# Kernel tuning notes

Hardware: AMD Instinct MI355X
Metric: run time of the kernel (lower is better)

Reference implementation:

```python
import jax, jax.numpy as jnp
import numpy as np

N_HEAD, D_K, D_V = 8, 32, 32
ATTN_MAX_DIST = 3
LN_EPS = 1e-6


def _layernorm(x, w, b):
    mu = jnp.mean(x, axis=-1, keepdims=True)
    var = jnp.mean(jnp.square(x - mu), axis=-1, keepdims=True)
    return (x - mu) * jax.lax.rsqrt(var + LN_EPS) * w + b


def setup_inputs() -> dict:
    key = jax.random.key(0)
    ks = jax.random.split(key, 8)
    B, E, D, PMAX = 4, 1500, 256, 5
    x = jax.random.normal(ks[0], (B, D, E), dtype=jnp.float32)
    dist_matrices = jax.random.randint(ks[1], (B, E, E), 0, 11, dtype=jnp.int32)
    s = 0.02
    Wq = jax.random.normal(ks[2], (D, N_HEAD * D_K), dtype=jnp.float32) * s
    Wk = jax.random.normal(ks[3], (D, N_HEAD * D_K), dtype=jnp.float32) * s
    Wv = jax.random.normal(ks[4], (D, N_HEAD * D_V), dtype=jnp.float32) * s
    Wfc = jax.random.normal(ks[5], (N_HEAD * D_V, D), dtype=jnp.float32) * s
    ln_w = jnp.ones((D,), dtype=jnp.float32)
    ln_b = jnp.zeros((D,), dtype=jnp.float32)
    base_rpr = jax.random.normal(ks[6], (PMAX + 1, D_K), dtype=jnp.float32) * s
    return {"x": x, "dist_matrices": dist_matrices, "Wq": Wq, "Wk": Wk,
            "Wv": Wv, "Wfc": Wfc, "ln_w": ln_w, "ln_b": ln_b, "base_rpr": base_rpr}


def reference(x, dist_matrices, Wq, Wk, Wv, Wfc, ln_w, ln_b, base_rpr):
    B, D, E = x.shape
    H, DK, DV = N_HEAD, D_K, D_V
    s = jnp.transpose(x, (0, 2, 1))          # [B, E, D]
    residual = s
    # NOTE: in the original, only q is layer-normed; k and v use raw input.
    qn = _layernorm(s, ln_w, ln_b)
    q = (qn @ Wq).reshape(B, E, H, DK).transpose(0, 2, 1, 3)   # [B,H,E,DK]
    k = (s @ Wk).reshape(B, E, H, DK).transpose(0, 2, 1, 3)
    v = (s @ Wv).reshape(B, E, H, DV).transpose(0, 2, 1, 3)
    qs = q / jnp.sqrt(jnp.asarray(DK, q.dtype))
    attn1 = jnp.einsum('bhqd,bhkd->bhqk', qs, k)               # [B,H,E,E]
    q_dot_rpr = jnp.einsum('bhqd,pd->bhqp', qs, base_rpr)      # [B,H,E,P+1]
    max_neighbor = base_rpr.shape[0] - 1
    idx = jnp.minimum(dist_matrices, max_neighbor)             # [B,E,E]
    idx4 = jnp.broadcast_to(idx[:, None], (B, H, E, E))
    attn2 = jnp.take_along_axis(q_dot_rpr, idx4, axis=-1)      # gather bias per edge pair
    attn = attn1 + attn2
    mask = dist_matrices <= ATTN_MAX_DIST                      # [B,E,E] local attention mask
    attn = jnp.where(mask[:, None], attn, jnp.asarray(-1e9, attn.dtype))
    attn = jax.nn.softmax(attn, axis=-1)                       # dropout=eval -> identity
    out = jnp.einsum('bhqk,bhkd->bhqd', attn, v)               # [B,H,E,DV]
    out = out.transpose(0, 2, 1, 3).reshape(B, E, H * DV)
    out = out @ Wfc + residual                                 # [B,E,D]
    x_out = jnp.transpose(out, (0, 2, 1))                      # [B,D,E]
    # attention-per-edge statistic (no grads in original: detached)
    m = mask[:, None].astype(attn.dtype)                       # [B,1,E,E]
    attn_sum = jnp.sum(jax.lax.stop_gradient(attn) * m, axis=(1, 2))  # [B,E]
    valid = jnp.sum(m, axis=(1, 2))                            # [B,E] (broadcasted over heads)
    attn_per_edge = attn_sum / valid
    return (x_out, attn, attn_per_edge)
```

## Files before the change

### kernel.cpp

```cpp
#include <hip/hip_runtime.h>


#define E_ 1500
#define D_ 256
#define HH 8
#define BB 4
#define MM (BB * E_)
#define KT_ 64
#define NKT_ 24

typedef float f32x4 __attribute__((ext_vector_type(4)));
typedef short short8 __attribute__((ext_vector_type(8)));

static __device__ inline unsigned short f2bf(float f) {
  unsigned u = __float_as_uint(f);
  unsigned r = (u + 0x7fff + ((u >> 16) & 1)) >> 16;
  return (unsigned short)r;
}
static __device__ inline float bf2f(unsigned short u) {
  return __uint_as_float(((unsigned)u) << 16);
}

__global__ __launch_bounds__(256) void t0_transpose(const float* __restrict__ x,
                                                    float* __restrict__ xt,
                                                    unsigned short* __restrict__ xtb) {
  __shared__ float tl[32][33];
  const int b = blockIdx.z;
  const int dt = blockIdx.x * 32;
  const int et = blockIdx.y * 32;
  const int tx = threadIdx.x, ty = threadIdx.y;
#pragma unroll
  for (int j = 0; j < 4; j++) {
    int d = dt + ty + j * 8;
    int e = et + tx;
    float v = 0.f;
    if (e < E_) v = x[(size_t)b * D_ * E_ + (size_t)d * E_ + e];
    tl[ty + j * 8][tx] = v;
  }
  __syncthreads();
#pragma unroll
  for (int j = 0; j < 4; j++) {
    int e = et + ty + j * 8;
    int d = dt + tx;
    if (e < E_) {
      float v = tl[tx][ty + j * 8];
      size_t idx = ((size_t)b * E_ + e) * D_ + d;
      xt[idx] = v;
      xtb[idx] = f2bf(v);
    }
  }
}

__global__ __launch_bounds__(256) void t1_wt(const float* __restrict__ Wq,
                                             const float* __restrict__ Wk,
                                             const float* __restrict__ Wv,
                                             const float* __restrict__ Wfc,
                                             unsigned short* __restrict__ WT) {
  __shared__ float tl[32][33];
  const int mat = blockIdx.z;
  const float* W = (mat == 0) ? Wq : (mat == 1) ? Wk : (mat == 2) ? Wv : Wfc;
  const int kt = blockIdx.x * 32, nt = blockIdx.y * 32;
  const int tx = threadIdx.x, ty = threadIdx.y;
#pragma unroll
  for (int j = 0; j < 4; j++)
    tl[ty + j * 8][tx] = W[(size_t)(kt + ty + j * 8) * 256 + nt + tx];
  __syncthreads();
#pragma unroll
  for (int j = 0; j < 4; j++)
    WT[(size_t)mat * 65536 + (size_t)(nt + ty + j * 8) * 256 + kt + tx] =
        f2bf(tl[tx][ty + j * 8]);
}

__global__ __launch_bounds__(256) void k1_ln(const float* __restrict__ xt,
                                             const float* __restrict__ lnw,
                                             const float* __restrict__ lnb,
                                             unsigned short* __restrict__ qnb) {
  const int m = blockIdx.x;
  const int t = threadIdx.x;
  float v = xt[(size_t)m * D_ + t];
  float s = v, s2 = v * v;
#pragma unroll
  for (int o = 1; o < 64; o <<= 1) {
    s += __shfl_xor(s, o);
    s2 += __shfl_xor(s2, o);
  }
  __shared__ float ps[4], ps2[4], mv[2];
  const int w = t >> 6;
  if ((t & 63) == 0) { ps[w] = s; ps2[w] = s2; }
  __syncthreads();
  if (t == 0) {
    float ts = ps[0] + ps[1] + ps[2] + ps[3];
    float ts2 = ps2[0] + ps2[1] + ps2[2] + ps2[3];
    float mu = ts * (1.f / 256.f);
    float var = ts2 * (1.f / 256.f) - mu * mu;
    mv[0] = mu;
    mv[1] = rsqrtf(var + 1e-6f);
  }
  __syncthreads();
  qnb[(size_t)m * D_ + t] = f2bf((v - mv[0]) * mv[1] * lnw[t] + lnb[t]);
}

__global__ __launch_bounds__(256) void kproj(
    const unsigned short* __restrict__ xtb, const unsigned short* __restrict__ qnb,
    const unsigned short* __restrict__ WT, unsigned short* __restrict__ qb,
    unsigned short* __restrict__ kb, unsigned short* __restrict__ vb) {
  const int mat = blockIdx.y >> 2;
  const int n0 = (blockIdx.y & 3) * 64;
  const int m0 = blockIdx.x * 64;
  const int t = threadIdx.x;
  const int w = t >> 6, l = t & 63, quad = l >> 4, l15 = l & 15;
  const unsigned short* A = (mat == 0) ? qnb : xtb;
  const unsigned short* B = WT + (size_t)mat * 65536;
  unsigned short* dst = (mat == 0) ? qb : ((mat == 1) ? kb : vb);
  const float scale = (mat == 0) ? 0.17677669529663687f : 1.0f;

  int mrow = m0 + w * 16 + l15;
  if (mrow > MM - 1) mrow = MM - 1;
  short8 af[8];
#pragma unroll
  for (int kc = 0; kc < 8; kc++)
    af[kc] = *(const short8*)(A + (size_t)mrow * 256 + kc * 32 + quad * 8);

#pragma unroll
  for (int ntile = 0; ntile < 4; ntile++) {
    const int n = n0 + ntile * 16 + l15;
    f32x4 acc = {0.f, 0.f, 0.f, 0.f};
#pragma unroll
    for (int kc = 0; kc < 8; kc++) {
      short8 bf = *(const short8*)(B + (size_t)n * 256 + kc * 32 + quad * 8);
      acc = __builtin_amdgcn_mfma_f32_16x16x32_bf16(af[kc], bf, acc, 0, 0, 0);
    }
#pragma unroll
    for (int r = 0; r < 4; r++) {
      int m = m0 + w * 16 + quad * 4 + r;
      if (m < MM) dst[(size_t)m * 256 + n] = f2bf(acc[r] * scale);
    }
  }
}

__global__ __launch_bounds__(512, 2) void k2_attn(
    const unsigned short* __restrict__ qb, const unsigned short* __restrict__ kb,
    const unsigned short* __restrict__ vb, const int* __restrict__ dist,
    const float* __restrict__ rpr, float* __restrict__ attn,
    unsigned short* __restrict__ aob, float* __restrict__ asum,
    float* __restrict__ validf) {
  __shared__ unsigned short vT[2][8][2312];
  __shared__ unsigned short pS[8][2312];
  __shared__ int distT[2][2816];
  __shared__ float qdrS[8][32][4];
  __shared__ float rinvS[8][32];

  const int blk = blockIdx.x;
  const int b = blk / 47;
  const int qt = blk % 47;
  const int q0 = qt * 32;
  const int t = threadIdx.x;
  const int w = t >> 6, l = t & 63, quad = l >> 4, l15 = l & 15;

#pragma unroll
  for (int ii = 0; ii < 2; ii++) {
    int id = t + ii * 512;
    int h = id >> 7, rem = id & 127, q = rem >> 2, p = rem & 3;
    int qg = q0 + q;
    float s = 0.f;
    if (qg < E_) {
      const unsigned short* qp = qb + ((size_t)(b * E_ + qg)) * 256 + h * 32;
      for (int d = 0; d < 32; d++) s += bf2f(qp[d]) * rpr[p * 32 + d];
    }
    qdrS[h][q][p] = s;
  }

  short8 aq[2];
#pragma unroll
  for (int qs = 0; qs < 2; qs++) {
    int qg = q0 + qs * 16 + l15;
    if (qg > E_ - 1) qg = E_ - 1;
    aq[qs] = *(const short8*)(qb + ((size_t)(b * E_ + qg)) * 256 + w * 32 + quad * 8);
  }

  float rs[2][4] = {{0.f, 0.f, 0.f, 0.f}, {0.f, 0.f, 0.f, 0.f}};
  f32x4 accPV[2][2];
#pragma unroll
  for (int qs = 0; qs < 2; qs++)
#pragma unroll
    for (int dv = 0; dv < 2; dv++) {
      f32x4 z = {0.f, 0.f, 0.f, 0.f};
      accPV[qs][dv] = z;
    }

  short8 kregA[4], kregB[4];

  auto loadD = [&](int kt) -> int4 {
    int qrow = t >> 4, c0 = (t & 15) * 4;
    int qg = q0 + qrow;
    int rq = qg < E_ ? qg : E_ - 1;
    int cb = kt * KT_ + c0;
    int cc2 = cb <= E_ - 4 ? cb : E_ - 4;
    return *(const int4*)(dist + ((size_t)b * E_ + rq) * (size_t)E_ + cc2);
  };
  auto writeD = [&](int kt, int buf, int4 d4) {
    int qrow = t >> 4, c0 = (t & 15) * 4;
    int qg = q0 + qrow;
    int cb = kt * KT_ + c0;
    int da[4] = {d4.x, d4.y, d4.z, d4.w};
#pragma unroll
    for (int j = 0; j < 4; j++) {
      int ok = (qg < E_) & ((cb + j) < E_);
      distT[buf][(c0 + j) * 44 + qrow] = ok ? da[j] : 8;
    }
  };
  auto loadV = [&](int kt, uint4 (&vr)[4]) {
    const int r = t >> 3, hh = t & 7;
    const int kg = kt * KT_ + r;
    const uint4 z = {0u, 0u, 0u, 0u};
    if (kg < E_) {
      const unsigned short* vp = vb + ((size_t)(b * E_ + kg)) * 256 + hh * 32;
      vr[0] = *(const uint4*)(vp);
      vr[1] = *(const uint4*)(vp + 8);
      vr[2] = *(const uint4*)(vp + 16);
      vr[3] = *(const uint4*)(vp + 24);
    } else {
      vr[0] = z; vr[1] = z; vr[2] = z; vr[3] = z;
    }
  };
  auto writeV = [&](int buf, const uint4 (&vr)[4]) {
    const int r = t >> 3, hh = t & 7;
    union { uint4 u[4]; unsigned short s[32]; } vv;
    vv.u[0] = vr[0]; vv.u[1] = vr[1]; vv.u[2] = vr[2]; vv.u[3] = vr[3];
#pragma unroll
    for (int j = 0; j < 32; j++) vT[buf][hh][j * 72 + r] = vv.s[j];
  };
  auto loadK = [&](int kt, short8 (&kr)[4]) {
#pragma unroll
    for (int ks = 0; ks < 4; ks++) {
      int kg = kt * KT_ + ks * 16 + l15;
      if (kg > E_ - 1) kg = E_ - 1;
      kr[ks] = *(const short8*)(kb + ((size_t)(b * E_ + kg)) * 256 + w * 32 + quad * 8);
    }
  };

  auto body1 = [&](int kt, short8 (&kcur)[4], short8 (&knxt)[4], int cur) {
    const int k0 = kt * KT_;
    const int nxt = cur ^ 1;
    const bool pf = (kt + 1) < NKT_;
    int4 d4;
    uint4 vr[4];
    if (pf) {
      d4 = loadD(kt + 1);
      loadV(kt + 1, vr);
      loadK(kt + 1, knxt);
    }
    int cc[4] = {0, 0, 0, 0};
#pragma unroll
    for (int qs = 0; qs < 2; qs++) {
#pragma unroll
      for (int ks = 0; ks < 4; ks++) {
        f32x4 z = {0.f, 0.f, 0.f, 0.f};
        f32x4 c = __builtin_amdgcn_mfma_f32_16x16x32_bf16(aq[qs], kcur[ks], z, 0, 0, 0);
        int4 dd4 = *(const int4*)&distT[cur][(ks * 16 + l15) * 44 + qs * 16 + quad * 4];
        int da[4] = {dd4.x, dd4.y, dd4.z, dd4.w};
#pragma unroll
        for (int r = 0; r < 4; r++) {
          int ql = qs * 16 + quad * 4 + r;
          float e = 0.f;
          if (da[r] <= 3) e = __expf(c[r] + qdrS[w][ql][da[r] & 3]);
          rs[qs][r] += e;
          pS[w][ql * 72 + ks * 16 + l15] = f2bf(e);
        }
        if (w == 0)
          cc[ks] += (da[0] <= 3) + (da[1] <= 3) + (da[2] <= 3) + (da[3] <= 3);
      }
    }
    if (w == 0) {
#pragma unroll
      for (int ks = 0; ks < 4; ks++) {
        int v = cc[ks];
        v += __shfl_xor(v, 16);
        v += __shfl_xor(v, 32);
        int kcol = k0 + ks * 16 + l15;
        if (quad == 0 && kcol < E_) atomicAdd(validf + b * E_ + kcol, (float)v);
      }
    }
#pragma unroll
    for (int kc = 0; kc < 2; kc++) {
      short8 bv0 = *(const short8*)&vT[cur][w][(l15) * 72 + kc * 32 + quad * 8];
      short8 bv1 = *(const short8*)&vT[cur][w][(16 + l15) * 72 + kc * 32 + quad * 8];
#pragma unroll
      for (int qs = 0; qs < 2; qs++) {
        short8 ap = *(const short8*)&pS[w][(qs * 16 + l15) * 72 + kc * 32 + quad * 8];
        accPV[qs][0] = __builtin_amdgcn_mfma_f32_16x16x32_bf16(ap, bv0, accPV[qs][0], 0, 0, 0);
        accPV[qs][1] = __builtin_amdgcn_mfma_f32_16x16x32_bf16(ap, bv1, accPV[qs][1], 0, 0, 0);
      }
    }
    if (pf) {
      writeD(kt + 1, nxt, d4);
      writeV(nxt, vr);
    }
    __syncthreads();
  };

  auto body2 = [&](int kt, short8 (&kcur)[4], short8 (&knxt)[4], int cur) {
    const int k0 = kt * KT_;
    const int nxt = cur ^ 1;
    const bool pf = (kt + 1) < NKT_;
    int4 d4;
    if (pf) {
      d4 = loadD(kt + 1);
      loadK(kt + 1, knxt);
    }
    float ca[4] = {0.f, 0.f, 0.f, 0.f};
    const size_t abase = ((size_t)(b * HH + w)) * E_;
#pragma unroll
    for (int qs = 0; qs < 2; qs++) {
#pragma unroll
      for (int ks = 0; ks < 4; ks++) {
        f32x4 z = {0.f, 0.f, 0.f, 0.f};
        f32x4 c = __builtin_amdgcn_mfma_f32_16x16x32_bf16(aq[qs], kcur[ks], z, 0, 0, 0);
        int4 dd4 = *(const int4*)&distT[cur][(ks * 16 + l15) * 44 + qs * 16 + quad * 4];
        int da[4] = {dd4.x, dd4.y, dd4.z, dd4.w};
        int kcol = k0 + ks * 16 + l15;
#pragma unroll
        for (int r = 0; r < 4; r++) {
          int ql = qs * 16 + quad * 4 + r;
          float p = 0.f;
          if (da[r] <= 3)
            p = __expf(c[r] + qdrS[w][ql][da[r] & 3]) * rinvS[w][ql];
          ca[ks] += p;
          int qg = q0 + ql;
          if (qg < E_ && kcol < E_) attn[(abase + qg) * E_ + kcol] = p;
        }
      }
    }
#pragma unroll
    for (int ks = 0; ks < 4; ks++) {
      float v = ca[ks];
      v += __shfl_xor(v, 16);
      v += __shfl_xor(v, 32);
      int kcol = k0 + ks * 16 + l15;
      if (quad == 0 && kcol < E_) atomicAdd(asum + b * E_ + kcol, v);
    }
    if (pf) writeD(kt + 1, nxt, d4);
    __syncthreads();
  };

  {
    int4 d4 = loadD(0);
    uint4 vr[4];
    loadV(0, vr);
    loadK(0, kregA);
    writeD(0, 0, d4);
    writeV(0, vr);
  }
  __syncthreads();
  for (int kt = 0; kt < NKT_; kt += 2) {
    body1(kt, kregA, kregB, 0);
    body1(kt + 1, kregB, kregA, 1);
  }

#pragma unroll
  for (int qs = 0; qs < 2; qs++)
#pragma unroll
    for (int r = 0; r < 4; r++) {
      float v = rs[qs][r];
      v += __shfl_xor(v, 1);
      v += __shfl_xor(v, 2);
      v += __shfl_xor(v, 4);
      v += __shfl_xor(v, 8);
      if (l15 == 0) rinvS[w][qs * 16 + quad * 4 + r] = v;
    }
  __syncthreads();
  if (t < 256) {
    int h = t >> 5, q = t & 31;
    float s = rinvS[h][q];
    rinvS[h][q] = (s > 0.f) ? 1.f / s : 0.f;
  }
  __syncthreads();

#pragma unroll
  for (int qs = 0; qs < 2; qs++)
#pragma unroll
    for (int dv = 0; dv < 2; dv++) {
      f32x4 a = accPV[qs][dv];
#pragma unroll
      for (int r = 0; r < 4; r++) {
        int ql = qs * 16 + quad * 4 + r;
        int qg = q0 + ql;
        if (qg < E_)
          aob[((size_t)(b * E_ + qg)) * 256 + w * 32 + dv * 16 + l15] =
              f2bf(a[r] * rinvS[w][ql]);
      }
    }

  {
    int4 d4 = loadD(0);
    loadK(0, kregA);
    writeD(0, 0, d4);
  }
  __syncthreads();
  for (int kt = 0; kt < NKT_; kt += 2) {
    body2(kt, kregA, kregB, 0);
    body2(kt + 1, kregB, kregA, 1);
  }
}

__global__ __launch_bounds__(256) void k_fc(const unsigned short* __restrict__ aob,
                                            const unsigned short* __restrict__ WT,
                                            const float* __restrict__ x,
                                            float* __restrict__ xout) {
  const int n0 = blockIdx.y * 64;
  const int m0 = blockIdx.x * 64;
  const int t = threadIdx.x;
  const int w = t >> 6, l = t & 63, quad = l >> 4, l15 = l & 15;
  const unsigned short* B = WT + (size_t)3 * 65536;

  int mrow = m0 + w * 16 + l15;
  if (mrow > MM - 1) mrow = MM - 1;
  short8 af[8];
#pragma unroll
  for (int kc = 0; kc < 8; kc++)
    af[kc] = *(const short8*)(aob + (size_t)mrow * 256 + kc * 32 + quad * 8);

#pragma unroll
  for (int ntile = 0; ntile < 4; ntile++) {
    const int nc = n0 + ntile * 16 + l15;
    f32x4 acc = {0.f, 0.f, 0.f, 0.f};
#pragma unroll
    for (int kc = 0; kc < 8; kc++) {
      short8 bf = *(const short8*)(B + (size_t)nc * 256 + kc * 32 + quad * 8);
      acc = __builtin_amdgcn_mfma_f32_16x16x32_bf16(af[kc], bf, acc, 0, 0, 0);
    }
    int m = m0 + w * 16 + quad * 4;
    if (m < MM) {
      int bb = m / E_, e = m - bb * E_;
      size_t idx = ((size_t)bb * 256 + nc) * E_ + e;
      float4 rx = *(const float4*)(x + idx);
      *(float4*)(xout + idx) = make_float4(acc[0] + rx.x, acc[1] + rx.y,
                                           acc[2] + rx.z, acc[3] + rx.w);
    }
  }
}

__global__ __launch_bounds__(256) void k5_div(const float* __restrict__ asum,
                                              const float* __restrict__ validf,
                                              float* __restrict__ ape) {
  int i = blockIdx.x * 256 + threadIdx.x;
  if (i < BB * E_) ape[i] = asum[i] / validf[i];
}

extern "C" void kernel_launch(void* const* d_in, const int* in_sizes, int n_in,
                              void* d_out, int out_size, void* d_ws,
                              size_t ws_size, hipStream_t stream) {
  const float* x = (const float*)d_in[0];
  const int* dist = (const int*)d_in[1];
  const float* Wq = (const float*)d_in[2];
  const float* Wk = (const float*)d_in[3];
  const float* Wv = (const float*)d_in[4];
  const float* Wfc = (const float*)d_in[5];
  const float* lnw = (const float*)d_in[6];
  const float* lnb = (const float*)d_in[7];
  const float* rpr = (const float*)d_in[8];

  float* out0 = (float*)d_out;
  float* attn = out0 + 1536000;
  float* ape = out0 + 73536000;

  float* ws = (float*)d_ws;
  float* xt = ws;
  unsigned short* xtb = (unsigned short*)(ws + 1536000);
  unsigned short* qnb = (unsigned short*)(ws + 2304000);
  unsigned short* qb = (unsigned short*)(ws + 3072000);
  unsigned short* kb = (unsigned short*)(ws + 3840000);
  unsigned short* vb = (unsigned short*)(ws + 4608000);
  unsigned short* aob = (unsigned short*)(ws + 5376000);
  unsigned short* WT = (unsigned short*)(ws + 6144000);
  float* asum = ws + 6275072;
  float* validf = ws + 6281072;

  hipMemsetAsync(asum, 0, 12000 * sizeof(float), stream);

  t0_transpose<<<dim3(8, 47, 4), dim3(32, 8), 0, stream>>>(x, xt, xtb);
  t1_wt<<<dim3(8, 8, 4), dim3(32, 8), 0, stream>>>(Wq, Wk, Wv, Wfc, WT);
  k1_ln<<<MM, 256, 0, stream>>>(xt, lnw, lnb, qnb);
  kproj<<<dim3(94, 12), 256, 0, stream>>>(xtb, qnb, WT, qb, kb, vb);
  k2_attn<<<188, 512, 0, stream>>>(qb, kb, vb, dist, rpr, attn, aob, asum,
                                   validf);
  k_fc<<<dim3(94, 4), 256, 0, stream>>>(aob, WT, x, out0);
  k5_div<<<24, 256, 0, stream>>>(asum, validf, ape);
}
```

Baseline: 629.0 us.

## Pack distance matrix into LDS nibbles, pre-transpose V, fuse transpose with layernorm

```diff
diff --git a/kernel.cpp b/kernel.cpp
--- a/kernel.cpp
+++ b/kernel.cpp
@@ -6,11 +6,12 @@
 #define HH 8
 #define BB 4
 #define MM (BB * E_)
-#define KT_ 64
 #define NKT_ 24
+#define VROW 1536
 
 typedef float f32x4 __attribute__((ext_vector_type(4)));
 typedef short short8 __attribute__((ext_vector_type(8)));
+typedef unsigned uint2v __attribute__((ext_vector_type(2)));
 
 static __device__ inline unsigned short f2bf(float f) {
   unsigned u = __float_as_uint(f);
@@ -21,32 +22,56 @@
   return __uint_as_float(((unsigned)u) << 16);
 }
 
-__global__ __launch_bounds__(256) void t0_transpose(const float* __restrict__ x,
-                                                    float* __restrict__ xt,
-                                                    unsigned short* __restrict__ xtb) {
-  __shared__ float tl[32][33];
-  const int b = blockIdx.z;
-  const int dt = blockIdx.x * 32;
-  const int et = blockIdx.y * 32;
-  const int tx = threadIdx.x, ty = threadIdx.y;
-#pragma unroll
-  for (int j = 0; j < 4; j++) {
-    int d = dt + ty + j * 8;
-    int e = et + tx;
-    float v = 0.f;
-    if (e < E_) v = x[(size_t)b * D_ * E_ + (size_t)d * E_ + e];
-    tl[ty + j * 8][tx] = v;
+__global__ __launch_bounds__(256) void t0ln(const float* __restrict__ x,
+                                            const float* __restrict__ lnw,
+                                            const float* __restrict__ lnb,
+                                            unsigned short* __restrict__ xtb,
+                                            unsigned short* __restrict__ qnb) {
+  __shared__ float tl[32][257];
+  const int b = blockIdx.y;
+  const int e0 = blockIdx.x * 32;
+  const int t = threadIdx.x;
+  const int tx = t & 31, ty8 = t >> 5;
+#pragma unroll
+  for (int dt = 0; dt < 8; dt++) {
+#pragma unroll
+    for (int j = 0; j < 4; j++) {
+      int d = dt * 32 + ty8 * 4 + j;
+      int e = e0 + tx;
+      float v = (e < E_) ? x[((size_t)b * D_ + d) * E_ + e] : 0.f;
+      tl[tx][d] = v;
+    }
   }
   __syncthreads();
-#pragma unroll
-  for (int j = 0; j < 4; j++) {
-    int e = et + ty + j * 8;
-    int d = dt + tx;
-    if (e < E_) {
-      float v = tl[tx][ty + j * 8];
-      size_t idx = ((size_t)b * E_ + e) * D_ + d;
-      xt[idx] = v;
-      xtb[idx] = f2bf(v);
+  const int er = t >> 3, seg = t & 7;
+  float s = 0.f, s2 = 0.f;
+#pragma unroll
+  for (int j = 0; j < 32; j++) {
+    float v = tl[er][seg + j * 8];
+    s += v;
+    s2 += v * v;
+  }
+  s += __shfl_xor(s, 1); s2 += __shfl_xor(s2, 1);
+  s += __shfl_xor(s, 2); s2 += __shfl_xor(s2, 2);
+  s += __shfl_xor(s, 4); s2 += __shfl_xor(s2, 4);
+  float mu = s * (1.f / 256.f);
+  float var = s2 * (1.f / 256.f) - mu * mu;
+  float rsig = rsqrtf(var + 1e-6f);
+  int eg = e0 + er;
+  if (eg < E_) {
+    size_t ro = ((size_t)b * E_ + eg) * 256;
+#pragma unroll
+    for (int g = 0; g < 4; g++) {
+      int d0 = seg * 32 + g * 8;
+      union { unsigned short u[8]; short8 v; } xs, qs8;
+#pragma unroll
+      for (int j = 0; j < 8; j++) {
+        float v = tl[er][d0 + j];
+        xs.u[j] = f2bf(v);
+        qs8.u[j] = f2bf((v - mu) * rsig * lnw[d0 + j] + lnb[d0 + j]);
+      }
+      *(short8*)(xtb + ro + d0) = xs.v;
+      *(short8*)(qnb + ro + d0) = qs8.v;
     }
   }
 }
@@ -71,39 +96,10 @@
         f2bf(tl[tx][ty + j * 8]);
 }
 
-__global__ __launch_bounds__(256) void k1_ln(const float* __restrict__ xt,
-                                             const float* __restrict__ lnw,
-                                             const float* __restrict__ lnb,
-                                             unsigned short* __restrict__ qnb) {
-  const int m = blockIdx.x;
-  const int t = threadIdx.x;
-  float v = xt[(size_t)m * D_ + t];
-  float s = v, s2 = v * v;
-#pragma unroll
-  for (int o = 1; o < 64; o <<= 1) {
-    s += __shfl_xor(s, o);
-    s2 += __shfl_xor(s2, o);
-  }
-  __shared__ float ps[4], ps2[4], mv[2];
-  const int w = t >> 6;
-  if ((t & 63) == 0) { ps[w] = s; ps2[w] = s2; }
-  __syncthreads();
-  if (t == 0) {
-    float ts = ps[0] + ps[1] + ps[2] + ps[3];
-    float ts2 = ps2[0] + ps2[1] + ps2[2] + ps2[3];
-    float mu = ts * (1.f / 256.f);
-    float var = ts2 * (1.f / 256.f) - mu * mu;
-    mv[0] = mu;
-    mv[1] = rsqrtf(var + 1e-6f);
-  }
-  __syncthreads();
-  qnb[(size_t)m * D_ + t] = f2bf((v - mv[0]) * mv[1] * lnw[t] + lnb[t]);
-}
-
 __global__ __launch_bounds__(256) void kproj(
     const unsigned short* __restrict__ xtb, const unsigned short* __restrict__ qnb,
     const unsigned short* __restrict__ WT, unsigned short* __restrict__ qb,
-    unsigned short* __restrict__ kb, unsigned short* __restrict__ vb) {
+    unsigned short* __restrict__ kb, unsigned short* __restrict__ vbt) {
   const int mat = blockIdx.y >> 2;
   const int n0 = (blockIdx.y & 3) * 64;
   const int m0 = blockIdx.x * 64;
@@ -111,7 +107,6 @@
   const int w = t >> 6, l = t & 63, quad = l >> 4, l15 = l & 15;
   const unsigned short* A = (mat == 0) ? qnb : xtb;
   const unsigned short* B = WT + (size_t)mat * 65536;
-  unsigned short* dst = (mat == 0) ? qb : ((mat == 1) ? kb : vb);
   const float scale = (mat == 0) ? 0.17677669529663687f : 1.0f;
 
   int mrow = m0 + w * 16 + l15;
@@ -130,25 +125,38 @@
       short8 bf = *(const short8*)(B + (size_t)n * 256 + kc * 32 + quad * 8);
       acc = __builtin_amdgcn_mfma_f32_16x16x32_bf16(af[kc], bf, acc, 0, 0, 0);
     }
-#pragma unroll
-    for (int r = 0; r < 4; r++) {
-      int m = m0 + w * 16 + quad * 4 + r;
-      if (m < MM) dst[(size_t)m * 256 + n] = f2bf(acc[r] * scale);
+    if (mat == 2) {
+      int m = m0 + w * 16 + quad * 4;
+      if (m < MM) {
+        int bb = m / E_, e0 = m - bb * E_;
+        uint2v uv;
+        uv.x = (unsigned)f2bf(acc[0]) | ((unsigned)f2bf(acc[1]) << 16);
+        uv.y = (unsigned)f2bf(acc[2]) | ((unsigned)f2bf(acc[3]) << 16);
+        *(uint2v*)(vbt + (size_t)((bb * 8 + (n >> 5)) * 32 + (n & 31)) * VROW +
+                   e0) = uv;
+      }
+    } else {
+      unsigned short* dst = (mat == 0) ? qb : kb;
+#pragma unroll
+      for (int r = 0; r < 4; r++) {
+        int m = m0 + w * 16 + quad * 4 + r;
+        if (m < MM) dst[(size_t)m * 256 + n] = f2bf(acc[r] * scale);
+      }
     }
   }
 }
 
 __global__ __launch_bounds__(512, 2) void k2_attn(
     const unsigned short* __restrict__ qb, const unsigned short* __restrict__ kb,
-    const unsigned short* __restrict__ vb, const int* __restrict__ dist,
+    const unsigned short* __restrict__ vbt, const int* __restrict__ dist,
     const float* __restrict__ rpr, float* __restrict__ attn,
     unsigned short* __restrict__ aob, float* __restrict__ asum,
     float* __restrict__ validf) {
-  __shared__ unsigned short vT[2][8][2312];
-  __shared__ unsigned short pS[8][2312];
-  __shared__ int distT[2][2816];
+  __shared__ __align__(16) unsigned short vT[2][8][32][72];
+  __shared__ __align__(16) unsigned short pS[8][2320];
+  __shared__ __align__(16) unsigned char distN[32][776];
   __shared__ float qdrS[8][32][4];
-  __shared__ float rinvS[8][32];
+  __shared__ float colacc[1544];
 
   const int blk = blockIdx.x;
   const int b = blk / 47;
@@ -156,6 +164,32 @@
   const int q0 = qt * 32;
   const int t = threadIdx.x;
   const int w = t >> 6, l = t & 63, quad = l >> 4, l15 = l & 15;
+
+  for (int idx = t; idx < 32 * 188; idx += 512) {
+    int row = idx / 188, wd = idx - row * 188;
+    int qg = q0 + row;
+    int k0 = wd * 8;
+    unsigned word = 0x88888888u;
+    if (qg < E_) {
+      const int* dp = dist + ((size_t)b * E_ + qg) * E_ + k0;
+      int4 a = *(const int4*)dp;
+      word = (unsigned)(a.x & 15) | ((unsigned)(a.y & 15) << 4) |
+             ((unsigned)(a.z & 15) << 8) | ((unsigned)(a.w & 15) << 12);
+      if (k0 + 8 <= E_) {
+        int4 c = *(const int4*)(dp + 4);
+        word |= ((unsigned)(c.x & 15) << 16) | ((unsigned)(c.y & 15) << 20) |
+                ((unsigned)(c.z & 15) << 24) | ((unsigned)(c.w & 15) << 28);
+      } else {
+        word |= 0x88880000u;
+      }
+    }
+    *(unsigned*)&distN[row][wd * 4] = word;
+  }
+  for (int idx = t; idx < 32 * 6; idx += 512) {
+    int row = idx / 6, wd = 188 + idx - (idx / 6) * 6;
+    *(unsigned*)&distN[row][wd * 4] = 0x88888888u;
+  }
+  for (int idx = t; idx < 1544; idx += 512) colacc[idx] = 0.f;
 
 #pragma unroll
   for (int ii = 0; ii < 2; ii++) {
@@ -178,113 +212,75 @@
     aq[qs] = *(const short8*)(qb + ((size_t)(b * E_ + qg)) * 256 + w * 32 + quad * 8);
   }
 
-  float rs[2][4] = {{0.f, 0.f, 0.f, 0.f}, {0.f, 0.f, 0.f, 0.f}};
-  f32x4 accPV[2][2];
-#pragma unroll
-  for (int qs = 0; qs < 2; qs++)
-#pragma unroll
-    for (int dv = 0; dv < 2; dv++) {
-      f32x4 z = {0.f, 0.f, 0.f, 0.f};
-      accPV[qs][dv] = z;
-    }
-
-  short8 kregA[4], kregB[4];
-
-  auto loadD = [&](int kt) -> int4 {
-    int qrow = t >> 4, c0 = (t & 15) * 4;
-    int qg = q0 + qrow;
-    int rq = qg < E_ ? qg : E_ - 1;
-    int cb = kt * KT_ + c0;
-    int cc2 = cb <= E_ - 4 ? cb : E_ - 4;
-    return *(const int4*)(dist + ((size_t)b * E_ + rq) * (size_t)E_ + cc2);
-  };
-  auto writeD = [&](int kt, int buf, int4 d4) {
-    int qrow = t >> 4, c0 = (t & 15) * 4;
-    int qg = q0 + qrow;
-    int cb = kt * KT_ + c0;
-    int da[4] = {d4.x, d4.y, d4.z, d4.w};
-#pragma unroll
-    for (int j = 0; j < 4; j++) {
-      int ok = (qg < E_) & ((cb + j) < E_);
-      distT[buf][(c0 + j) * 44 + qrow] = ok ? da[j] : 8;
+  const unsigned short* kbase = kb + (size_t)b * E_ * 256 + w * 32 + quad * 8;
+  const int vrr = t >> 1, vh = vrr >> 5, vdv = vrr & 31, vc0 = (t & 1) * 32;
+  const unsigned short* vsrc = vbt + (size_t)((b * 8 + vh) * 32 + vdv) * VROW + vc0;
+
+  auto loadK = [&](int kt, short8 (&kf)[4]) {
+#pragma unroll
+    for (int ks = 0; ks < 4; ks++) {
+      int kg = kt * 64 + ks * 16 + l15;
+      if (kg > E_ - 1) kg = E_ - 1;
+      kf[ks] = *(const short8*)(kbase + (size_t)kg * 256);
     }
   };
   auto loadV = [&](int kt, uint4 (&vr)[4]) {
-    const int r = t >> 3, hh = t & 7;
-    const int kg = kt * KT_ + r;
-    const uint4 z = {0u, 0u, 0u, 0u};
-    if (kg < E_) {
-      const unsigned short* vp = vb + ((size_t)(b * E_ + kg)) * 256 + hh * 32;
-      vr[0] = *(const uint4*)(vp);
-      vr[1] = *(const uint4*)(vp + 8);
-      vr[2] = *(const uint4*)(vp + 16);
-      vr[3] = *(const uint4*)(vp + 24);
-    } else {
-      vr[0] = z; vr[1] = z; vr[2] = z; vr[3] = z;
-    }
+#pragma unroll
+    for (int j = 0; j < 4; j++) vr[j] = *(const uint4*)(vsrc + kt * 64 + j * 8);
   };
   auto writeV = [&](int buf, const uint4 (&vr)[4]) {
-    const int r = t >> 3, hh = t & 7;
-    union { uint4 u[4]; unsigned short s[32]; } vv;
-    vv.u[0] = vr[0]; vv.u[1] = vr[1]; vv.u[2] = vr[2]; vv.u[3] = vr[3];
-#pragma unroll
-    for (int j = 0; j < 32; j++) vT[buf][hh][j * 72 + r] = vv.s[j];
+    uint4* dst = (uint4*)&vT[buf][vh][vdv][vc0];
+#pragma unroll
+    for (int j = 0; j < 4; j++) dst[j] = vr[j];
   };
-  auto loadK = [&](int kt, short8 (&kr)[4]) {
-#pragma unroll
-    for (int ks = 0; ks < 4; ks++) {
-      int kg = kt * KT_ + ks * 16 + l15;
-      if (kg > E_ - 1) kg = E_ - 1;
-      kr[ks] = *(const short8*)(kb + ((size_t)(b * E_ + kg)) * 256 + w * 32 + quad * 8);
-    }
-  };
-
-  auto body1 = [&](int kt, short8 (&kcur)[4], short8 (&knxt)[4], int cur) {
-    const int k0 = kt * KT_;
-    const int nxt = cur ^ 1;
-    const bool pf = (kt + 1) < NKT_;
-    int4 d4;
+
+  short8 kA[4], kB[4];
+  f32x4 accPV[2][2];
+#pragma unroll
+  for (int qs = 0; qs < 2; qs++)
+#pragma unroll
+    for (int dvh = 0; dvh < 2; dvh++) {
+      f32x4 z = {0.f, 0.f, 0.f, 0.f};
+      accPV[qs][dvh] = z;
+    }
+  float rs[2][4] = {{0.f, 0.f, 0.f, 0.f}, {0.f, 0.f, 0.f, 0.f}};
+
+  {
     uint4 vr[4];
-    if (pf) {
-      d4 = loadD(kt + 1);
-      loadV(kt + 1, vr);
-      loadK(kt + 1, knxt);
-    }
-    int cc[4] = {0, 0, 0, 0};
+    loadV(0, vr);
+    loadK(0, kA);
+    writeV(0, vr);
+  }
+  __syncthreads();
+
+  auto body1 = [&](int kt, short8 (&kf)[4], short8 (&kn)[4], int cur) {
+    const int ktn = (kt + 1 < NKT_) ? kt + 1 : kt;
+    uint4 vr[4];
+    loadV(ktn, vr);
+    loadK(ktn, kn);
+    const int kl0 = kt * 64;
 #pragma unroll
     for (int qs = 0; qs < 2; qs++) {
 #pragma unroll
       for (int ks = 0; ks < 4; ks++) {
         f32x4 z = {0.f, 0.f, 0.f, 0.f};
-        f32x4 c = __builtin_amdgcn_mfma_f32_16x16x32_bf16(aq[qs], kcur[ks], z, 0, 0, 0);
-        int4 dd4 = *(const int4*)&distT[cur][(ks * 16 + l15) * 44 + qs * 16 + quad * 4];
-        int da[4] = {dd4.x, dd4.y, dd4.z, dd4.w};
+        f32x4 c = __builtin_amdgcn_mfma_f32_16x16x32_bf16(aq[qs], kf[ks], z, 0, 0, 0);
+        const int kcol = kl0 + ks * 16 + l15;
 #pragma unroll
         for (int r = 0; r < 4; r++) {
           int ql = qs * 16 + quad * 4 + r;
+          int dd = (distN[ql][kcol >> 1] >> ((kcol & 1) * 4)) & 15;
           float e = 0.f;
-          if (da[r] <= 3) e = __expf(c[r] + qdrS[w][ql][da[r] & 3]);
+          if (dd <= 3) e = __expf(c[r] + qdrS[w][ql][dd & 3]);
           rs[qs][r] += e;
           pS[w][ql * 72 + ks * 16 + l15] = f2bf(e);
         }
-        if (w == 0)
-          cc[ks] += (da[0] <= 3) + (da[1] <= 3) + (da[2] <= 3) + (da[3] <= 3);
-      }
-    }
-    if (w == 0) {
-#pragma unroll
-      for (int ks = 0; ks < 4; ks++) {
-        int v = cc[ks];
-        v += __shfl_xor(v, 16);
-        v += __shfl_xor(v, 32);
-        int kcol = k0 + ks * 16 + l15;
-        if (quad == 0 && kcol < E_) atomicAdd(validf + b * E_ + kcol, (float)v);
       }
     }
 #pragma unroll
     for (int kc = 0; kc < 2; kc++) {
-      short8 bv0 = *(const short8*)&vT[cur][w][(l15) * 72 + kc * 32 + quad * 8];
-      short8 bv1 = *(const short8*)&vT[cur][w][(16 + l15) * 72 + kc * 32 + quad * 8];
+      short8 bv0 = *(const short8*)&vT[cur][w][l15][kc * 32 + quad * 8];
+      short8 bv1 = *(const short8*)&vT[cur][w][16 + l15][kc * 32 + quad * 8];
 #pragma unroll
       for (int qs = 0; qs < 2; qs++) {
         short8 ap = *(const short8*)&pS[w][(qs * 16 + l15) * 72 + kc * 32 + quad * 8];
@@ -292,71 +288,16 @@
         accPV[qs][1] = __builtin_amdgcn_mfma_f32_16x16x32_bf16(ap, bv1, accPV[qs][1], 0, 0, 0);
       }
     }
-    if (pf) {
-      writeD(kt + 1, nxt, d4);
-      writeV(nxt, vr);
-    }
+    writeV(cur ^ 1, vr);
     __syncthreads();
   };
 
-  auto body2 = [&](int kt, short8 (&kcur)[4], short8 (&knxt)[4], int cur) {
-    const int k0 = kt * KT_;
-    const int nxt = cur ^ 1;
-    const bool pf = (kt + 1) < NKT_;
-    int4 d4;
-    if (pf) {
-      d4 = loadD(kt + 1);
-      loadK(kt + 1, knxt);
-    }
-    float ca[4] = {0.f, 0.f, 0.f, 0.f};
-    const size_t abase = ((size_t)(b * HH + w)) * E_;
-#pragma unroll
-    for (int qs = 0; qs < 2; qs++) {
-#pragma unroll
-      for (int ks = 0; ks < 4; ks++) {
-        f32x4 z = {0.f, 0.f, 0.f, 0.f};
-        f32x4 c = __builtin_amdgcn_mfma_f32_16x16x32_bf16(aq[qs], kcur[ks], z, 0, 0, 0);
-        int4 dd4 = *(const int4*)&distT[cur][(ks * 16 + l15) * 44 + qs * 16 + quad * 4];
-        int da[4] = {dd4.x, dd4.y, dd4.z, dd4.w};
-        int kcol = k0 + ks * 16 + l15;
-#pragma unroll
-        for (int r = 0; r < 4; r++) {
-          int ql = qs * 16 + quad * 4 + r;
-          float p = 0.f;
-          if (da[r] <= 3)
-            p = __expf(c[r] + qdrS[w][ql][da[r] & 3]) * rinvS[w][ql];
-          ca[ks] += p;
-          int qg = q0 + ql;
-          if (qg < E_ && kcol < E_) attn[(abase + qg) * E_ + kcol] = p;
-        }
-      }
-    }
-#pragma unroll
-    for (int ks = 0; ks < 4; ks++) {
-      float v = ca[ks];
-      v += __shfl_xor(v, 16);
-      v += __shfl_xor(v, 32);
-      int kcol = k0 + ks * 16 + l15;
-      if (quad == 0 && kcol < E_) atomicAdd(asum + b * E_ + kcol, v);
-    }
-    if (pf) writeD(kt + 1, nxt, d4);
-    __syncthreads();
-  };
-
-  {
-    int4 d4 = loadD(0);
-    uint4 vr[4];
-    loadV(0, vr);
-    loadK(0, kregA);
-    writeD(0, 0, d4);
-    writeV(0, vr);
-  }
-  __syncthreads();
   for (int kt = 0; kt < NKT_; kt += 2) {
-    body1(kt, kregA, kregB, 0);
-    body1(kt + 1, kregB, kregA, 1);
-  }
-
+    body1(kt, kA, kB, 0);
+    body1(kt + 1, kB, kA, 1);
+  }
+
+  float rinv[2][4];
 #pragma unroll
   for (int qs = 0; qs < 2; qs++)
 #pragma unroll
@@ -366,47 +307,81 @@
       v += __shfl_xor(v, 2);
       v += __shfl_xor(v, 4);
       v += __shfl_xor(v, 8);
-      if (l15 == 0) rinvS[w][qs * 16 + quad * 4 + r] = v;
-    }
-  __syncthreads();
-  if (t < 256) {
-    int h = t >> 5, q = t & 31;
-    float s = rinvS[h][q];
-    rinvS[h][q] = (s > 0.f) ? 1.f / s : 0.f;
-  }
-  __syncthreads();
+      rinv[qs][r] = (v > 0.f) ? 1.f / v : 0.f;
+    }
 
 #pragma unroll
   for (int qs = 0; qs < 2; qs++)
 #pragma unroll
-    for (int dv = 0; dv < 2; dv++) {
-      f32x4 a = accPV[qs][dv];
+    for (int dvh = 0; dvh < 2; dvh++) {
+      f32x4 a = accPV[qs][dvh];
 #pragma unroll
       for (int r = 0; r < 4; r++) {
         int ql = qs * 16 + quad * 4 + r;
         int qg = q0 + ql;
         if (qg < E_)
-          aob[((size_t)(b * E_ + qg)) * 256 + w * 32 + dv * 16 + l15] =
-              f2bf(a[r] * rinvS[w][ql]);
-      }
-    }
-
-  {
-    int4 d4 = loadD(0);
-    loadK(0, kregA);
-    writeD(0, 0, d4);
-  }
+          aob[((size_t)(b * E_ + qg)) * 256 + w * 32 + dvh * 16 + l15] =
+              f2bf(a[r] * rinv[qs][r]);
+      }
+    }
+
+  if (w == 0) {
+    for (int c = l; c < E_; c += 64) {
+      int cnt = 0;
+#pragma unroll
+      for (int r = 0; r < 32; r++)
+        cnt += (((distN[r][c >> 1] >> ((c & 1) * 4)) & 15) <= 3);
+      atomicAdd(validf + b * E_ + c, 8.f * (float)cnt);
+    }
+  }
+
+  loadK(0, kA);
+  auto body2 = [&](int kt, short8 (&kf)[4], short8 (&kn)[4]) {
+    const int ktn = (kt + 1 < NKT_) ? kt + 1 : kt;
+    loadK(ktn, kn);
+    const int kl0 = kt * 64;
+#pragma unroll
+    for (int ks = 0; ks < 4; ks++) {
+      const int kcol = kl0 + ks * 16 + l15;
+      const bool kok = kcol < E_;
+      float cs = 0.f;
+#pragma unroll
+      for (int qs = 0; qs < 2; qs++) {
+        f32x4 z = {0.f, 0.f, 0.f, 0.f};
+        f32x4 c = __builtin_amdgcn_mfma_f32_16x16x32_bf16(aq[qs], kf[ks], z, 0, 0, 0);
+#pragma unroll
+        for (int r = 0; r < 4; r++) {
+          int ql = qs * 16 + quad * 4 + r;
+          int dd = (distN[ql][kcol >> 1] >> ((kcol & 1) * 4)) & 15;
+          float p = 0.f;
+          if (dd <= 3) p = __expf(c[r] + qdrS[w][ql][dd & 3]) * rinv[qs][r];
+          cs += p;
+          int qg = q0 + ql;
+          if (qg < E_ && kok)
+            attn[((size_t)(b * 8 + w) * E_ + qg) * E_ + kcol] = p;
+        }
+      }
+      cs += __shfl_xor(cs, 16);
+      cs += __shfl_xor(cs, 32);
+      if (quad == 0 && kok) atomicAdd(&colacc[kl0 + ks * 16 + l15], cs);
+    }
+  };
+
+  for (int kt = 0; kt < NKT_; kt += 2) {
+    body2(kt, kA, kB);
+    body2(kt + 1, kB, kA);
+  }
+
   __syncthreads();
-  for (int kt = 0; kt < NKT_; kt += 2) {
-    body2(kt, kregA, kregB, 0);
-    body2(kt + 1, kregB, kregA, 1);
-  }
+  for (int idx = t; idx < E_; idx += 512)
+    atomicAdd(asum + b * E_ + idx, colacc[idx]);
 }
 
 __global__ __launch_bounds__(256) void k_fc(const unsigned short* __restrict__ aob,
                                             const unsigned short* __restrict__ WT,
                                             const float* __restrict__ x,
                                             float* __restrict__ xout) {
+  __shared__ float tl[64][65];
   const int n0 = blockIdx.y * 64;
   const int m0 = blockIdx.x * 64;
   const int t = threadIdx.x;
@@ -422,20 +397,34 @@
 
 #pragma unroll
   for (int ntile = 0; ntile < 4; ntile++) {
-    const int nc = n0 + ntile * 16 + l15;
+    const int nl = ntile * 16 + l15;
     f32x4 acc = {0.f, 0.f, 0.f, 0.f};
 #pragma unroll
     for (int kc = 0; kc < 8; kc++) {
-      short8 bf = *(const short8*)(B + (size_t)nc * 256 + kc * 32 + quad * 8);
+      short8 bf = *(const short8*)(B + (size_t)(n0 + nl) * 256 + kc * 32 + quad * 8);
       acc = __builtin_amdgcn_mfma_f32_16x16x32_bf16(af[kc], bf, acc, 0, 0, 0);
     }
-    int m = m0 + w * 16 + quad * 4;
+    const int ml = w * 16 + quad * 4;
+#pragma unroll
+    for (int r = 0; r < 4; r++) tl[ml + r][nl] = acc[r];
+  }
+  __syncthreads();
+  const int nl = t >> 2;
+  const int e0l = (t & 3) * 16;
+  const int nc = n0 + nl;
+#pragma unroll
+  for (int i = 0; i < 4; i++) {
+    int m = m0 + e0l + i * 4;
     if (m < MM) {
-      int bb = m / E_, e = m - bb * E_;
+      int bb = m / E_;
+      int e = m - bb * E_;
       size_t idx = ((size_t)bb * 256 + nc) * E_ + e;
       float4 rx = *(const float4*)(x + idx);
-      *(float4*)(xout + idx) = make_float4(acc[0] + rx.x, acc[1] + rx.y,
-                                           acc[2] + rx.z, acc[3] + rx.w);
+      float4 v = make_float4(tl[e0l + i * 4 + 0][nl] + rx.x,
+                             tl[e0l + i * 4 + 1][nl] + rx.y,
+                             tl[e0l + i * 4 + 2][nl] + rx.z,
+                             tl[e0l + i * 4 + 3][nl] + rx.w);
+      *(float4*)(xout + idx) = v;
     }
   }
 }
@@ -465,24 +454,23 @@
   float* ape = out0 + 73536000;
 
   float* ws = (float*)d_ws;
-  float* xt = ws;
-  unsigned short* xtb = (unsigned short*)(ws + 1536000);
-  unsigned short* qnb = (unsigned short*)(ws + 2304000);
-  unsigned short* qb = (unsigned short*)(ws + 3072000);
-  unsigned short* kb = (unsigned short*)(ws + 3840000);
-  unsigned short* vb = (unsigned short*)(ws + 4608000);
-  unsigned short* aob = (unsigned short*)(ws + 5376000);
-  unsigned short* WT = (unsigned short*)(ws + 6144000);
-  float* asum = ws + 6275072;
-  float* validf = ws + 6281072;
+  unsigned short* xtb = (unsigned short*)ws;
+  unsigned short* qnb = (unsigned short*)(ws + 768000);
+  unsigned short* qb = (unsigned short*)(ws + 1536000);
+  unsigned short* kb = (unsigned short*)(ws + 2304000);
+  unsigned short* vbt = (unsigned short*)(ws + 3072000);
+  unsigned short* aob = (unsigned short*)(ws + 3858432);
+  unsigned short* WT = (unsigned short*)(ws + 4626432);
+  float* asum = ws + 4757504;
+  float* validf = ws + 4763504;
 
   hipMemsetAsync(asum, 0, 12000 * sizeof(float), stream);
-
-  t0_transpose<<<dim3(8, 47, 4), dim3(32, 8), 0, stream>>>(x, xt, xtb);
+  hipMemsetAsync(vbt, 0, 1572864 * sizeof(unsigned short), stream);
+
+  t0ln<<<dim3(47, 4), 256, 0, stream>>>(x, lnw, lnb, xtb, qnb);
   t1_wt<<<dim3(8, 8, 4), dim3(32, 8), 0, stream>>>(Wq, Wk, Wv, Wfc, WT);
-  k1_ln<<<MM, 256, 0, stream>>>(xt, lnw, lnb, qnb);
-  kproj<<<dim3(94, 12), 256, 0, stream>>>(xtb, qnb, WT, qb, kb, vb);
-  k2_attn<<<188, 512, 0, stream>>>(qb, kb, vb, dist, rpr, attn, aob, asum,
+  kproj<<<dim3(94, 12), 256, 0, stream>>>(xtb, qnb, WT, qb, kb, vbt);
+  k2_attn<<<188, 512, 0, stream>>>(qb, kb, vbt, dist, rpr, attn, aob, asum,
                                    validf);
   k_fc<<<dim3(94, 4), 256, 0, stream>>>(aob, WT, x, out0);
   k5_div<<<24, 256, 0, stream>>>(asum, validf, ape);
```

After: 585.7 us. 6.9% less time.
